# Performance work log

Measured on AMD Instinct MI355X. Metric: run time of the kernel, lower is better.

## Reference

```python
import jax, jax.numpy as jnp
import numpy as np

EPS_ATTN = 1e-5   # LinearCrossAttention eps
EPS_LN = 1e-5     # LayerNorm default eps


def _rot_interleaved(t):
    # rotate_half=False path of timm apply_rot_embed_cat: interleaved pairs
    t1 = t[..., ::2]
    t2 = t[..., 1::2]
    return jnp.stack([-t2, t1], axis=-1).reshape(t.shape)


def _apply_rope_cat(t, rope):
    # rope: [N_r, 2*D] = concat(sin, cos); t: [B, H, N_r, D]
    sin, cos = jnp.split(rope, 2, axis=-1)  # each [N_r, D]
    return t * cos + _rot_interleaved(t) * sin


def _layer_norm(x, g, b):
    m = jnp.mean(x, axis=-1, keepdims=True)
    v = jnp.var(x, axis=-1, keepdims=True)
    return (x - m) * jax.lax.rsqrt(v + EPS_LN) * g + b


def setup_inputs() -> dict:
    key = jax.random.key(0)
    ks = jax.random.split(key, 4)
    B, N, C = 8, 4096, 768
    H, D = 12, 64
    npt = 1
    x = jax.random.normal(ks[0], (B, N, C), dtype=jnp.float32)
    rope = jax.random.normal(ks[1], (N - npt, 2 * D), dtype=jnp.float32)
    qkv_w = jax.random.normal(ks[2], (3 * C, C), dtype=jnp.float32) * (C ** -0.5)
    proj_w = jax.random.normal(ks[3], (C, C), dtype=jnp.float32) * (C ** -0.5)
    return {
        "x": x,
        "rope": rope,
        "qkv_w": qkv_w,
        "q_bias": jnp.zeros((C,), jnp.float32),
        "v_bias": jnp.zeros((C,), jnp.float32),
        "norm_g": jnp.ones((C,), jnp.float32),
        "norm_b": jnp.zeros((C,), jnp.float32),
        "proj_w": proj_w,
        "proj_b": jnp.zeros((C,), jnp.float32),
        "num_heads": 12,
        "num_prefix_tokens": 1,
    }


def reference(x, rope, qkv_w, q_bias, v_bias, norm_g, norm_b, proj_w, proj_b,
              num_heads, num_prefix_tokens):
    B, N, C = x.shape
    H = num_heads
    D = C // H
    npt = num_prefix_tokens

    # fused qkv projection; k_bias is a zero buffer
    qkv_bias = jnp.concatenate([q_bias, jnp.zeros_like(q_bias), v_bias])
    qkv = x @ qkv_w.T + qkv_bias                      # [B, N, 3C]
    qkv = qkv.reshape(B, N, 3, H, D).transpose(2, 0, 3, 1, 4)  # [3, B, H, N, D]
    q, k, v = qkv[0], qkv[1], qkv[2]

    # RoPE on non-prefix tokens
    q = jnp.concatenate([q[:, :, :npt], _apply_rope_cat(q[:, :, npt:], rope)], axis=2)
    k = jnp.concatenate([k[:, :, :npt], _apply_rope_cat(k[:, :, npt:], rope)], axis=2)

    # linear cross-attention with tied softmax feature map
    phi_q = jax.nn.softmax(q, axis=-1)                # [B, H, N, D]
    phi_k = jax.nn.softmax(k, axis=-1)                # [B, H, N, D]
    kv = jnp.einsum('bhnd,bhne->bhde', phi_k, v)      # [B, H, D, D]
    z = jnp.einsum('bhnd,bhd->bhn', phi_q, phi_k.sum(axis=2))  # [B, H, N]
    out = jnp.einsum('bhnd,bhde->bhne', phi_q, kv) / (z[..., None] + EPS_ATTN)

    out = out.transpose(0, 2, 1, 3).reshape(B, N, C)  # [B, N, C]
    out = _layer_norm(out, norm_g, norm_b)            # scale_norm
    out = out @ proj_w.T + proj_b
    return out
```

## Files before the change

### kernel.cpp

```cpp
#include <hip/hip_runtime.h>
#include <stdint.h>


typedef __attribute__((ext_vector_type(8))) short short8;
typedef __attribute__((ext_vector_type(4))) float floatx4;

#define SPLIT_A 16
#define TILES_PER_BLK (32 / SPLIT_A)

#define SBAR()  do { asm volatile("" ::: "memory"); __builtin_amdgcn_s_barrier(); asm volatile("" ::: "memory"); } while (0)
#define LGKM0() do { asm volatile("s_waitcnt lgkmcnt(0)" ::: "memory"); __builtin_amdgcn_sched_barrier(0); } while (0)
#define WAITV6() asm volatile("s_waitcnt vmcnt(6)" ::: "memory")
#define WAITV0() asm volatile("s_waitcnt vmcnt(0)" ::: "memory")

__device__ __forceinline__ float b2f(unsigned short u) {
  union { unsigned int i; float f; } v; v.i = ((unsigned int)u) << 16; return v.f;
}
__device__ __forceinline__ unsigned short f2b(float f) {
  union { float f; unsigned int i; } v; v.f = f;
  unsigned int i = v.i;
  unsigned int r = (i + 0x7FFFu + ((i >> 16) & 1u)) >> 16;
  return (unsigned short)r;
}
__device__ __forceinline__ void unpack2(unsigned int u, float& a, float& b) {
  union { unsigned int i; float f; } x, y;
  x.i = u << 16; y.i = u & 0xFFFF0000u;
  a = x.f; b = y.f;
}

__device__ __forceinline__ void stage16(const void* g, void* l) {
#if defined(__has_builtin) && __has_builtin(__builtin_amdgcn_global_load_lds)
  __builtin_amdgcn_global_load_lds(
      (const __attribute__((address_space(1))) unsigned int*)g,
      (__attribute__((address_space(3))) unsigned int*)l, 16, 0, 0);
#else
  *(uint4*)l = *(const uint4*)g;
#endif
}

__global__ __launch_bounds__(256) void f32_to_bf16(
    const float* __restrict__ in, unsigned short* __restrict__ out, int n) {
  const int i = (blockIdx.x * 256 + threadIdx.x) * 8;
  if (i + 7 < n) {
    float4 a = *(const float4*)(in + i);
    float4 b = *(const float4*)(in + i + 4);
    unsigned short tmp[8] = {f2b(a.x), f2b(a.y), f2b(a.z), f2b(a.w),
                             f2b(b.x), f2b(b.y), f2b(b.z), f2b(b.w)};
    *(uint4*)(out + i) = *(uint4*)tmp;
  }
}

__global__ __launch_bounds__(256) void prep(
    const float* __restrict__ w, const float* __restrict__ pw,
    const float* __restrict__ qb, const float* __restrict__ vb,
    const float* __restrict__ pb,
    unsigned short* __restrict__ wbf, unsigned short* __restrict__ pwbf,
    float* __restrict__ qkvb, float* __restrict__ projb) {
  const int blk = blockIdx.x, t = threadIdx.x;
  if (blk < 1152) {
    const float* src = (blk < 864) ? w : pw;
    unsigned short* dst = (blk < 864) ? wbf : pwbf;
    const int i = ((blk < 864 ? blk : blk - 864) * 256 + t) * 8;
    float4 a = *(const float4*)(src + i);
    float4 b = *(const float4*)(src + i + 4);
    unsigned short tmp[8] = {f2b(a.x), f2b(a.y), f2b(a.z), f2b(a.w),
                             f2b(b.x), f2b(b.y), f2b(b.z), f2b(b.w)};
    *(uint4*)(dst + i) = *(uint4*)tmp;
  } else {
    const int i = (blk - 1152) * 256 + t;
    if (i < 2304) qkvb[i] = (i < 768) ? qb[i] : (i >= 1536 ? vb[i - 1536] : 0.f);
    if (i < 768) projb[i] = pb[i];
  }
}

template <int OUT_BF16>
__global__ __launch_bounds__(512, 2) void gemm256(
    const unsigned short* __restrict__ A, const unsigned short* __restrict__ W,
    const float* __restrict__ bias, void* __restrict__ Out,
    int K, int Nout, int nbn, int NT) {
  extern __shared__ __align__(16) unsigned short lds[];
  const int nwg = gridDim.x;
  const int orig = blockIdx.x;
  const int wg = (orig & 7) * (nwg >> 3) + (orig >> 3);
  const int bm = wg / nbn, bn = wg - bm * nbn;
  const int t = threadIdx.x;
  const int lane = t & 63, wave = t >> 6;
  const int wr = wave >> 2, wc = wave & 3;
  const int mr = lane & 15, kq8 = lane >> 4;

  const int rh0 = t >> 3, sl0 = t & 7;
  const size_t growA = (size_t)bm * 256;
  const size_t growB = (size_t)bn * 256;

  #define STAGE_HALF(buf, op, G, grow, k0, half)                               \
    do {                                                                       \
      const int row0_ = (half)*128 + rh0;                                      \
      const int row1_ = row0_ + 64;                                            \
      const unsigned short* s0_ =                                              \
          (G) + ((grow) + row0_) * (size_t)K + (k0) + ((sl0 ^ (row0_ & 7)) * 8);\
      const unsigned short* s1_ =                                              \
          (G) + ((grow) + row1_) * (size_t)K + (k0) + ((sl0 ^ (row1_ & 7)) * 8);\
      unsigned short* d0_ = lds + (buf)*32768 + (op)*16384 + (half)*8192 + t*8;\
      stage16(s0_, d0_);                                                       \
      stage16(s1_, d0_ + 4096);                                                \
    } while (0)

  floatx4 acc[8][4] = {};
  short8 afr[4][2], bfr[4][2];

  #define RD_A(buf, i, kk)                                                     \
    (*(const short8*)&lds[(buf)*32768 + (wr*128 + (i)*16 + mr)*64 +            \
        ((((kk)*4 + kq8) ^ ((wr*128 + (i)*16 + mr) & 7)) * 8)])
  #define RD_B(buf, j, kk)                                                     \
    (*(const short8*)&lds[(buf)*32768 + 16384 + (wc*64 + (j)*16 + mr)*64 +     \
        ((((kk)*4 + kq8) ^ ((wc*64 + (j)*16 + mr) & 7)) * 8)])

  #define QUAD(ih, jh)                                                         \
    do {                                                                       \
      __builtin_amdgcn_s_setprio(1);                                           \
      _Pragma("unroll")                                                        \
      for (int i_ = 0; i_ < 4; i_++)                                           \
        _Pragma("unroll")                                                      \
        for (int jr_ = 0; jr_ < 2; jr_++)                                      \
          _Pragma("unroll")                                                    \
          for (int kk_ = 0; kk_ < 2; kk_++)                                    \
            acc[(ih)*4 + i_][(jh)*2 + jr_] =                                   \
                __builtin_amdgcn_mfma_f32_16x16x32_bf16(                       \
                    afr[i_][kk_], bfr[(jh)*2 + jr_][kk_],                      \
                    acc[(ih)*4 + i_][(jh)*2 + jr_], 0, 0, 0);                  \
      __builtin_amdgcn_s_setprio(0);                                           \
    } while (0)

  STAGE_HALF(0, 0, A, growA, 0, 0);
  STAGE_HALF(0, 0, A, growA, 0, 1);
  STAGE_HALF(0, 1, W, growB, 0, 0);
  STAGE_HALF(0, 1, W, growB, 0, 1);
  STAGE_HALF(1, 1, W, growB, 64, 0);
  STAGE_HALF(1, 1, W, growB, 64, 1);
  STAGE_HALF(1, 0, A, growA, 64, 0);
  WAITV6();
  SBAR();

  const int NI = NT >> 1;
  for (int it = 0; it < NI; ++it) {
    const int ta = 2 * it, tb = ta + 1;
    const int kA = (ta + 2) * 64, kB = (tb + 2) * 64;
    const bool gA = (ta + 2) < NT, gB = (tb + 2) < NT;
#pragma unroll
    for (int i = 0; i < 4; i++) { afr[i][0] = RD_A(0, i, 0); afr[i][1] = RD_A(0, i, 1); }
#pragma unroll
    for (int j = 0; j < 4; j++) { bfr[j][0] = RD_B(0, j, 0); bfr[j][1] = RD_B(0, j, 1); }
    STAGE_HALF(1, 0, A, growA, tb * 64, 1);
    SBAR(); LGKM0();
    QUAD(0, 0);
    SBAR();
    if (gA) STAGE_HALF(0, 1, W, growB, kA, 0);
    SBAR();
    QUAD(0, 1);
    SBAR();
#pragma unroll
    for (int i = 0; i < 4; i++) { afr[i][0] = RD_A(0, i + 4, 0); afr[i][1] = RD_A(0, i + 4, 1); }
    if (gA) STAGE_HALF(0, 1, W, growB, kA, 1);
    SBAR(); LGKM0();
    QUAD(1, 0);
    SBAR();
    if (gA) STAGE_HALF(0, 0, A, growA, kA, 0);
    SBAR();
    QUAD(1, 1);
    if (gA) WAITV6(); else WAITV0();
    SBAR();
#pragma unroll
    for (int i = 0; i < 4; i++) { afr[i][0] = RD_A(1, i, 0); afr[i][1] = RD_A(1, i, 1); }
#pragma unroll
    for (int j = 0; j < 4; j++) { bfr[j][0] = RD_B(1, j, 0); bfr[j][1] = RD_B(1, j, 1); }
    if (gA) STAGE_HALF(0, 0, A, growA, kA, 1);
    SBAR(); LGKM0();
    QUAD(0, 0);
    SBAR();
    if (gB) STAGE_HALF(1, 1, W, growB, kB, 0);
    SBAR();
    QUAD(0, 1);
    SBAR();
#pragma unroll
    for (int i = 0; i < 4; i++) { afr[i][0] = RD_A(1, i + 4, 0); afr[i][1] = RD_A(1, i + 4, 1); }
    if (gB) STAGE_HALF(1, 1, W, growB, kB, 1);
    SBAR(); LGKM0();
    QUAD(1, 0);
    SBAR();
    if (gB) STAGE_HALF(1, 0, A, growA, kB, 0);
    SBAR();
    QUAD(1, 1);
    if (gB) WAITV6(); else WAITV0();
    SBAR();
  }

  const int mr4 = (lane >> 4) * 4, nc = lane & 15;
#pragma unroll
  for (int j = 0; j < 4; j++) {
    const int gc = bn * 256 + wc * 64 + j * 16 + nc;
    const float bv = bias[gc];
#pragma unroll
    for (int i = 0; i < 8; i++) {
      const int gr0 = bm * 256 + wr * 128 + i * 16 + mr4;
#pragma unroll
      for (int r = 0; r < 4; r++) {
        float v = acc[i][j][r] + bv;
        if (OUT_BF16)
          ((unsigned short*)Out)[(size_t)(gr0 + r) * Nout + gc] = f2b(v);
        else
          ((float*)Out)[(size_t)(gr0 + r) * Nout + gc] = v;
      }
    }
  }
  #undef STAGE_HALF
  #undef RD_A
  #undef RD_B
  #undef QUAD
}

__global__ __launch_bounds__(256) void pass_a(
    const unsigned short* __restrict__ qkv, const float* __restrict__ rope,
    float* __restrict__ kvP) {
  __shared__ float sphi[128 * 65];
  __shared__ __align__(16) unsigned short sv[128 * 64];
  const int bh = blockIdx.x, b = bh / 12, h = bh % 12;
  const int sp = blockIdx.y;
  const int t = threadIdx.x;
  const int lane = t & 63, wave = t >> 6;
  const int dg = lane >> 2;
  const int eg = lane & 3;
  float acc[4][16] = {};
  float ks4[4] = {};

  const int tile0 = sp * TILES_PER_BLK;
  for (int tile = tile0; tile < tile0 + TILES_PER_BLK; tile++) {
    __syncthreads();
    if (t < 128) {
      const int n = tile * 128 + t;
      const size_t rowb = (size_t)(b * 4096 + n) * 2304;
      const unsigned short* kp = qkv + rowb + 768 + h * 64;
      float kk[64];
#pragma unroll
      for (int c = 0; c < 8; c++) {
        uint4 u = *(const uint4*)(kp + c * 8);
        unpack2(u.x, kk[c * 8 + 0], kk[c * 8 + 1]);
        unpack2(u.y, kk[c * 8 + 2], kk[c * 8 + 3]);
        unpack2(u.z, kk[c * 8 + 4], kk[c * 8 + 5]);
        unpack2(u.w, kk[c * 8 + 6], kk[c * 8 + 7]);
      }
      if (n > 0) {
        const float* rp = rope + (size_t)(n - 1) * 128;
#pragma unroll
        for (int c = 0; c < 8; c++) {
          float sn[8], cs[8];
          *(float4*)&sn[0] = *(const float4*)(rp + c * 8);
          *(float4*)&sn[4] = *(const float4*)(rp + c * 8 + 4);
          *(float4*)&cs[0] = *(const float4*)(rp + 64 + c * 8);
          *(float4*)&cs[4] = *(const float4*)(rp + 64 + c * 8 + 4);
#pragma unroll
          for (int i = 0; i < 4; i++) {
            float e = kk[c * 8 + 2 * i], o = kk[c * 8 + 2 * i + 1];
            kk[c * 8 + 2 * i] = e * cs[2 * i] - o * sn[2 * i];
            kk[c * 8 + 2 * i + 1] = o * cs[2 * i + 1] + e * sn[2 * i + 1];
          }
        }
      }
      float mx = kk[0];
#pragma unroll
      for (int i = 1; i < 64; i++) mx = fmaxf(mx, kk[i]);
      float s = 0.f;
#pragma unroll
      for (int i = 0; i < 64; i++) { float e = __expf(kk[i] - mx); kk[i] = e; s += e; }
      const float inv = 1.f / s;
#pragma unroll
      for (int d = 0; d < 64; d++) sphi[t * 65 + d] = kk[d] * inv;
      const unsigned short* vp = qkv + rowb + 1536 + h * 64;
#pragma unroll
      for (int c = 0; c < 8; c++)
        *(uint4*)&sv[t * 64 + c * 8] = *(const uint4*)(vp + c * 8);
    }
    __syncthreads();
    const int n0 = wave * 32;
    for (int nn = n0; nn < n0 + 32; nn++) {
      float p[4];
#pragma unroll
      for (int i = 0; i < 4; i++) p[i] = sphi[nn * 65 + dg * 4 + i];
#pragma unroll
      for (int i = 0; i < 4; i++) ks4[i] += p[i];
      float vv[16];
      {
        uint4 u0 = *(const uint4*)&sv[nn * 64 + eg * 16];
        uint4 u1 = *(const uint4*)&sv[nn * 64 + eg * 16 + 8];
        unpack2(u0.x, vv[0], vv[1]);   unpack2(u0.y, vv[2], vv[3]);
        unpack2(u0.z, vv[4], vv[5]);   unpack2(u0.w, vv[6], vv[7]);
        unpack2(u1.x, vv[8], vv[9]);   unpack2(u1.y, vv[10], vv[11]);
        unpack2(u1.z, vv[12], vv[13]); unpack2(u1.w, vv[14], vv[15]);
      }
#pragma unroll
      for (int i = 0; i < 4; i++)
#pragma unroll
        for (int j = 0; j < 16; j++)
          acc[i][j] += p[i] * vv[j];
    }
  }

  __syncthreads();
  float* sred = sphi;
  float* o = kvP + ((size_t)bh * SPLIT_A + sp) * 4160;
#pragma unroll
  for (int half = 0; half < 2; half++) {
    if (wave != 0) {
      float* row = &sred[((wave - 1) * 64 + lane) * 33];
#pragma unroll
      for (int i = 0; i < 4; i++)
#pragma unroll
        for (int jj = 0; jj < 8; jj++) row[i * 8 + jj] = acc[i][half * 8 + jj];
    }
    __syncthreads();
    if (wave == 0) {
#pragma unroll
      for (int jj = 0; jj < 8; jj++) {
        float4 s4;
        float sv4[4];
#pragma unroll
        for (int i = 0; i < 4; i++) {
          float s = acc[i][half * 8 + jj];
#pragma unroll
          for (int w = 0; w < 3; w++) s += sred[(w * 64 + lane) * 33 + i * 8 + jj];
          sv4[i] = s;
        }
        s4.x = sv4[0]; s4.y = sv4[1]; s4.z = sv4[2]; s4.w = sv4[3];
        const int e = eg * 16 + half * 8 + jj;
        *(float4*)&o[e * 64 + dg * 4] = s4;
      }
    }
    __syncthreads();
  }
  if (wave != 0) {
#pragma unroll
    for (int i = 0; i < 4; i++) sred[((wave - 1) * 64 + lane) * 5 + i] = ks4[i];
  }
  __syncthreads();
  if (wave == 0 && eg == 0) {
    float4 s4;
    float sv4[4];
#pragma unroll
    for (int i = 0; i < 4; i++) {
      float s = ks4[i];
#pragma unroll
      for (int w = 0; w < 3; w++) s += sred[(w * 64 + lane) * 5 + i];
      sv4[i] = s;
    }
    s4.x = sv4[0]; s4.y = sv4[1]; s4.z = sv4[2]; s4.w = sv4[3];
    *(float4*)&o[4096 + dg * 4] = s4;
  }
}

__global__ __launch_bounds__(256) void reduce_kv(
    const float* __restrict__ kvP, float* __restrict__ kvG) {
  const int i = blockIdx.x * 256 + threadIdx.x;
  if (i >= 96 * 4160) return;
  const int bh = i / 4160, r = i - bh * 4160;
  const float* p = kvP + (size_t)bh * SPLIT_A * 4160 + r;
  float s = 0.f;
#pragma unroll
  for (int sp = 0; sp < SPLIT_A; sp++) s += p[(size_t)sp * 4160];
  kvG[i] = s;
}

__global__ __launch_bounds__(256) void pass_b(
    const unsigned short* __restrict__ qkv, const float* __restrict__ rope,
    const float* __restrict__ kvG, unsigned short* __restrict__ attn) {
  __shared__ __align__(16) unsigned short sp_[256 * 64];
  __shared__ __align__(16) unsigned short skv[64 * 64];
  __shared__ float szi[256];
  __shared__ float sks[64];
  const int bh = blockIdx.x, b = bh / 12, h = bh % 12;
  const int t = threadIdx.x;
  const float* kvb = kvG + (size_t)bh * 4160;

  {
    const int e = t >> 2, q = t & 3;
    const float* src = kvb + e * 64 + q * 16;
    unsigned short tmp[16];
#pragma unroll
    for (int i = 0; i < 16; i++) tmp[i] = f2b(src[i]);
    *(uint4*)&skv[e * 64 + (((q * 2) ^ (e & 7)) * 8)] = *(uint4*)&tmp[0];
    *(uint4*)&skv[e * 64 + (((q * 2 + 1) ^ (e & 7)) * 8)] = *(uint4*)&tmp[8];
  }
  if (t < 64) sks[t] = kvb[4096 + t];
  __syncthreads();

  const int n = blockIdx.y * 256 + t;
  const size_t rowb = (size_t)(b * 4096 + n) * 2304;
  const unsigned short* qp = qkv + rowb + h * 64;
  float ph[64];
#pragma unroll
  for (int c = 0; c < 8; c++) {
    uint4 u = *(const uint4*)(qp + c * 8);
    unpack2(u.x, ph[c * 8 + 0], ph[c * 8 + 1]);
    unpack2(u.y, ph[c * 8 + 2], ph[c * 8 + 3]);
    unpack2(u.z, ph[c * 8 + 4], ph[c * 8 + 5]);
    unpack2(u.w, ph[c * 8 + 6], ph[c * 8 + 7]);
  }
  if (n > 0) {
    const float* rp = rope + (size_t)(n - 1) * 128;
#pragma unroll
    for (int c = 0; c < 8; c++) {
      float sn[8], cs[8];
      *(float4*)&sn[0] = *(const float4*)(rp + c * 8);
      *(float4*)&sn[4] = *(const float4*)(rp + c * 8 + 4);
      *(float4*)&cs[0] = *(const float4*)(rp + 64 + c * 8);
      *(float4*)&cs[4] = *(const float4*)(rp + 64 + c * 8 + 4);
#pragma unroll
      for (int i = 0; i < 4; i++) {
        float e = ph[c * 8 + 2 * i], o = ph[c * 8 + 2 * i + 1];
        ph[c * 8 + 2 * i] = e * cs[2 * i] - o * sn[2 * i];
        ph[c * 8 + 2 * i + 1] = o * cs[2 * i + 1] + e * sn[2 * i + 1];
      }
    }
  }
  float mx = ph[0];
#pragma unroll
  for (int i = 1; i < 64; i++) mx = fmaxf(mx, ph[i]);
  float s = 0.f;
#pragma unroll
  for (int i = 0; i < 64; i++) { float e = __expf(ph[i] - mx); ph[i] = e; s += e; }
  const float inv = 1.f / s;
  float z = 0.f;
#pragma unroll
  for (int i = 0; i < 64; i++) { ph[i] *= inv; z += ph[i] * sks[i]; }
  szi[t] = 1.f / (z + 1e-5f);

#pragma unroll
  for (int sl = 0; sl < 8; sl += 2) {
    unsigned short tmp[16];
#pragma unroll
    for (int i = 0; i < 16; i++) tmp[i] = f2b(ph[sl * 8 + i]);
    *(uint4*)&sp_[t * 64 + ((sl ^ (t & 7)) * 8)] = *(uint4*)&tmp[0];
    *(uint4*)&sp_[t * 64 + (((sl + 1) ^ (t & 7)) * 8)] = *(uint4*)&tmp[8];
  }
  __syncthreads();

  const int lane = t & 63, wv = t >> 6;
  const int fr = lane & 15, fq = lane >> 4;
  floatx4 acc[4][4] = {};
#pragma unroll
  for (int kk = 0; kk < 2; kk++) {
    short8 kvf[4], pf[4];
#pragma unroll
    for (int j = 0; j < 4; j++) {
      const int e = j * 16 + fr;
      kvf[j] = *(const short8*)&skv[e * 64 + (((kk * 4 + fq) ^ (e & 7)) * 8)];
    }
#pragma unroll
    for (int i = 0; i < 4; i++) {
      const int tok = wv * 64 + i * 16 + fr;
      pf[i] = *(const short8*)&sp_[tok * 64 + (((kk * 4 + fq) ^ (tok & 7)) * 8)];
    }
#pragma unroll
    for (int i = 0; i < 4; i++)
#pragma unroll
      for (int j = 0; j < 4; j++)
        acc[i][j] = __builtin_amdgcn_mfma_f32_16x16x32_bf16(kvf[j], pf[i], acc[i][j], 0, 0, 0);
  }

#pragma unroll
  for (int i = 0; i < 4; i++) {
    const int tokl = wv * 64 + i * 16 + fr;
    const float zi = szi[tokl];
    unsigned short* orow =
        attn + (size_t)(b * 4096 + blockIdx.y * 256 + tokl) * 768 + h * 64;
#pragma unroll
    for (int j = 0; j < 4; j++) {
      const int e0 = j * 16 + fq * 4;
      unsigned short pk[4] = {f2b(acc[i][j][0] * zi), f2b(acc[i][j][1] * zi),
                              f2b(acc[i][j][2] * zi), f2b(acc[i][j][3] * zi)};
      *(uint2*)(orow + e0) = *(const uint2*)pk;
    }
  }
}

__global__ __launch_bounds__(256) void ln_kernel(
    unsigned short* __restrict__ buf, const float* __restrict__ g,
    const float* __restrict__ be) {
  const int row = blockIdx.x;
  const int t = threadIdx.x;
  unsigned short* p = buf + (size_t)row * 768;
  const float x0 = b2f(p[t]), x1 = b2f(p[t + 256]), x2 = b2f(p[t + 512]);
  float s = x0 + x1 + x2;
  float ss = x0 * x0 + x1 * x1 + x2 * x2;
#pragma unroll
  for (int m = 1; m < 64; m <<= 1) { s += __shfl_xor(s, m); ss += __shfl_xor(ss, m); }
  __shared__ float red[8];
  const int wave = t >> 6, lane = t & 63;
  if (lane == 0) { red[wave] = s; red[4 + wave] = ss; }
  __syncthreads();
  s = red[0] + red[1] + red[2] + red[3];
  ss = red[4] + red[5] + red[6] + red[7];
  const float mean = s * (1.f / 768.f);
  const float var = ss * (1.f / 768.f) - mean * mean;
  const float rsq = rsqrtf(var + 1e-5f);
  p[t] = f2b((x0 - mean) * rsq * g[t] + be[t]);
  p[t + 256] = f2b((x1 - mean) * rsq * g[t + 256] + be[t + 256]);
  p[t + 512] = f2b((x2 - mean) * rsq * g[t + 512] + be[t + 512]);
}

extern "C" void kernel_launch(void* const* d_in, const int* in_sizes, int n_in,
                              void* d_out, int out_size, void* d_ws, size_t ws_size,
                              hipStream_t stream) {
  (void)in_sizes; (void)n_in; (void)out_size; (void)ws_size;
  const float* x      = (const float*)d_in[0];
  const float* rope   = (const float*)d_in[1];
  const float* qkv_w  = (const float*)d_in[2];
  const float* q_bias = (const float*)d_in[3];
  const float* v_bias = (const float*)d_in[4];
  const float* norm_g = (const float*)d_in[5];
  const float* norm_b = (const float*)d_in[6];
  const float* proj_w = (const float*)d_in[7];
  const float* proj_b = (const float*)d_in[8];

  char* ws = (char*)d_ws;
  unsigned short* qkv  = (unsigned short*)ws;
  unsigned short* attn = (unsigned short*)(ws + 150994944);
  unsigned short* xbf  = attn;
  float* kvP   = (float*)(ws + 150994944);
  float* kvG   = (float*)(ws + 201326592);
  float* qkvb  = (float*)(ws + 202924032);
  float* projb = (float*)(ws + 202933248);
  unsigned short* wbf  = (unsigned short*)(ws + 202936320);
  unsigned short* pwbf = (unsigned short*)(ws + 206475264);

  hipFuncSetAttribute(reinterpret_cast<const void*>(&gemm256<1>),
                      hipFuncAttributeMaxDynamicSharedMemorySize, 131072);
  hipFuncSetAttribute(reinterpret_cast<const void*>(&gemm256<0>),
                      hipFuncAttributeMaxDynamicSharedMemorySize, 131072);

  f32_to_bf16<<<dim3(12288), dim3(256), 0, stream>>>(x, xbf, 25165824);
  prep<<<dim3(1161), dim3(256), 0, stream>>>(qkv_w, proj_w, q_bias, v_bias,
                                             proj_b, wbf, pwbf, qkvb, projb);
  gemm256<1><<<dim3(1152), dim3(512), 131072, stream>>>(xbf, wbf, qkvb, qkv,
                                                        768, 2304, 9, 12);
  pass_a<<<dim3(96, SPLIT_A), dim3(256), 0, stream>>>(qkv, rope, kvP);
  reduce_kv<<<dim3(1560), dim3(256), 0, stream>>>(kvP, kvG);
  pass_b<<<dim3(96, 16), dim3(256), 0, stream>>>(qkv, rope, kvG, attn);
  ln_kernel<<<dim3(32768), dim3(256), 0, stream>>>(attn, norm_g, norm_b);
  gemm256<0><<<dim3(384), dim3(512), 131072, stream>>>(attn, pwbf, projb, d_out,
                                                       768, 768, 3, 12);
}
```

Measured before the change: 594.0 us.

## Stage QKV GEMM epilogue through LDS and use smaller-tile GEMM for projection

The QKV GEMM swaps MFMA operand order so each lane holds four consecutive output columns. It then writes bf16 results with bias into a swizzled LDS tile and stores them to global memory as coalesced 16-byte rows, replacing scattered 2-byte stores. The output projection moves to a new simple 128x128-tile GEMM with 1536 blocks instead of 384, for better occupancy across CUs. The new projection kernel has no software pipelining, so its per-iteration efficiency may be lower.

```diff
diff --git a/kernel.cpp b/kernel.cpp
--- a/kernel.cpp
+++ b/kernel.cpp
@@ -73,10 +73,9 @@
   }
 }
 
-template <int OUT_BF16>
 __global__ __launch_bounds__(512, 2) void gemm256(
     const unsigned short* __restrict__ A, const unsigned short* __restrict__ W,
-    const float* __restrict__ bias, void* __restrict__ Out,
+    const float* __restrict__ bias, unsigned short* __restrict__ Out,
     int K, int Nout, int nbn, int NT) {
   extern __shared__ __align__(16) unsigned short lds[];
   const int nwg = gridDim.x;
@@ -126,7 +125,7 @@
           for (int kk_ = 0; kk_ < 2; kk_++)                                    \
             acc[(ih)*4 + i_][(jh)*2 + jr_] =                                   \
                 __builtin_amdgcn_mfma_f32_16x16x32_bf16(                       \
-                    afr[i_][kk_], bfr[(jh)*2 + jr_][kk_],                      \
+                    bfr[(jh)*2 + jr_][kk_], afr[i_][kk_],                      \
                     acc[(ih)*4 + i_][(jh)*2 + jr_], 0, 0, 0);                  \
       __builtin_amdgcn_s_setprio(0);                                           \
     } while (0)
@@ -194,14 +193,85 @@
     SBAR();
   }
 
+  const int fr = lane & 15, fq4 = (lane >> 4) * 4;
+#pragma unroll
+  for (int i = 0; i < 8; i++) {
+    const int lrow = wr * 128 + i * 16 + fr;
+#pragma unroll
+    for (int j = 0; j < 4; j++) {
+      const int colu = wc * 64 + j * 16 + fq4;
+      const float4 bv = *(const float4*)&bias[bn * 256 + colu];
+      unsigned short pk[4] = {f2b(acc[i][j][0] + bv.x), f2b(acc[i][j][1] + bv.y),
+                              f2b(acc[i][j][2] + bv.z), f2b(acc[i][j][3] + bv.w)};
+      const int chunk = colu >> 3;
+      const int low = colu & 7;
+      *(uint2*)&lds[lrow * 256 + ((chunk ^ (lrow & 7)) << 3) + low] =
+          *(const uint2*)pk;
+    }
+  }
+  SBAR();
+#pragma unroll
+  for (int p = 0; p < 16; p++) {
+    const int row = p * 16 + (t >> 5);
+    const int chunk = t & 31;
+    uint4 v = *(const uint4*)&lds[row * 256 + ((chunk ^ (row & 7)) << 3)];
+    *(uint4*)(Out + (size_t)(bm * 256 + row) * Nout + bn * 256 + chunk * 8) = v;
+  }
+  #undef STAGE_HALF
+  #undef RD_A
+  #undef RD_B
+  #undef QUAD
+}
+
+template <int OUT_BF16>
+__global__ __launch_bounds__(256) void gemm_bt(
+    const unsigned short* __restrict__ A, const unsigned short* __restrict__ W,
+    const float* __restrict__ bias, void* __restrict__ Out,
+    int M, int K, int Nout, int nbn) {
+  __shared__ __align__(16) unsigned short sA[128 * 32];
+  __shared__ __align__(16) unsigned short sB[128 * 32];
+  const int nwg = gridDim.x;
+  const int orig = blockIdx.x;
+  const int wg = (orig & 7) * (nwg >> 3) + (orig >> 3);
+  const int bm = wg / nbn;
+  const int bn = wg - bm * nbn;
+  const int t = threadIdx.x;
+  const int lane = t & 63, wave = t >> 6;
+  const int wm = (wave >> 1) * 64, wn = (wave & 1) * 64;
+  const int lr = t >> 2;
+  const int lc = (t & 3) * 8;
+  const size_t baseA = (size_t)(bm * 128 + lr) * K + lc;
+  const size_t baseB = (size_t)(bn * 128 + lr) * K + lc;
+  floatx4 acc[4][4] = {};
+
+  const int mr = lane & 15, kq = (lane >> 4) * 8;
+  for (int k0 = 0; k0 < K; k0 += 32) {
+    stage16(A + baseA + k0, &sA[t * 8]);
+    stage16(A + baseA + (size_t)64 * K + k0, &sA[2048 + t * 8]);
+    stage16(W + baseB + k0, &sB[t * 8]);
+    stage16(W + baseB + (size_t)64 * K + k0, &sB[2048 + t * 8]);
+    __syncthreads();
+    short8 af[4], bfr[4];
+#pragma unroll
+    for (int i = 0; i < 4; i++) af[i] = *(const short8*)&sA[(wm + i * 16 + mr) * 32 + kq];
+#pragma unroll
+    for (int j = 0; j < 4; j++) bfr[j] = *(const short8*)&sB[(wn + j * 16 + mr) * 32 + kq];
+#pragma unroll
+    for (int i = 0; i < 4; i++)
+#pragma unroll
+      for (int j = 0; j < 4; j++)
+        acc[i][j] = __builtin_amdgcn_mfma_f32_16x16x32_bf16(af[i], bfr[j], acc[i][j], 0, 0, 0);
+    __syncthreads();
+  }
+
   const int mr4 = (lane >> 4) * 4, nc = lane & 15;
 #pragma unroll
   for (int j = 0; j < 4; j++) {
-    const int gc = bn * 256 + wc * 64 + j * 16 + nc;
+    const int gc = bn * 128 + wn + j * 16 + nc;
     const float bv = bias[gc];
 #pragma unroll
-    for (int i = 0; i < 8; i++) {
-      const int gr0 = bm * 256 + wr * 128 + i * 16 + mr4;
+    for (int i = 0; i < 4; i++) {
+      const int gr0 = bm * 128 + wm + i * 16 + mr4;
 #pragma unroll
       for (int r = 0; r < 4; r++) {
         float v = acc[i][j][r] + bv;
@@ -212,10 +282,6 @@
       }
     }
   }
-  #undef STAGE_HALF
-  #undef RD_A
-  #undef RD_B
-  #undef QUAD
 }
 
 __global__ __launch_bounds__(256) void pass_a(
@@ -531,20 +597,18 @@
   unsigned short* wbf  = (unsigned short*)(ws + 202936320);
   unsigned short* pwbf = (unsigned short*)(ws + 206475264);
 
-  hipFuncSetAttribute(reinterpret_cast<const void*>(&gemm256<1>),
-                      hipFuncAttributeMaxDynamicSharedMemorySize, 131072);
-  hipFuncSetAttribute(reinterpret_cast<const void*>(&gemm256<0>),
+  hipFuncSetAttribute(reinterpret_cast<const void*>(&gemm256),
                       hipFuncAttributeMaxDynamicSharedMemorySize, 131072);
 
   f32_to_bf16<<<dim3(12288), dim3(256), 0, stream>>>(x, xbf, 25165824);
   prep<<<dim3(1161), dim3(256), 0, stream>>>(qkv_w, proj_w, q_bias, v_bias,
                                              proj_b, wbf, pwbf, qkvb, projb);
-  gemm256<1><<<dim3(1152), dim3(512), 131072, stream>>>(xbf, wbf, qkvb, qkv,
-                                                        768, 2304, 9, 12);
+  gemm256<<<dim3(1152), dim3(512), 131072, stream>>>(xbf, wbf, qkvb, qkv,
+                                                     768, 2304, 9, 12);
   pass_a<<<dim3(96, SPLIT_A), dim3(256), 0, stream>>>(qkv, rope, kvP);
   reduce_kv<<<dim3(1560), dim3(256), 0, stream>>>(kvP, kvG);
   pass_b<<<dim3(96, 16), dim3(256), 0, stream>>>(qkv, rope, kvG, attn);
   ln_kernel<<<dim3(32768), dim3(256), 0, stream>>>(attn, norm_g, norm_b);
-  gemm256<0><<<dim3(384), dim3(512), 131072, stream>>>(attn, pwbf, projb, d_out,
-                                                       768, 768, 3, 12);
-}
+  gemm_bt<0><<<dim3(1536), dim3(256), 0, stream>>>(attn, pwbf, projb, d_out,
+                                                   32768, 768, 768, 6);
+}
```

Result: faster. 562.1 us (-5.4%).
